# Performance work log

Measured on AMD Instinct MI355X. Metric: run time of the kernel, lower is better.

Reference implementation:

```python
import jax, jax.numpy as jnp
import numpy as np

BS, SL, D, NH = 2, 2048, 1024, 16
HD = D // NH
SCALE = D ** (-0.5)  # NOTE: source scales by full model dim, not head dim


def setup_inputs() -> dict:
    key = jax.random.key(0)
    k1, k2, k3 = jax.random.split(key, 3)
    return {
        "input_sequence": jax.random.normal(k1, (BS, SL, D), dtype=jnp.float32),
        "w_qkv": jax.random.normal(k2, (D, 3 * D), dtype=jnp.float32) * (D ** -0.5),
        "w_out": jax.random.normal(k3, (D, D), dtype=jnp.float32) * (D ** -0.5),
    }


def reference(input_sequence, w_qkv, w_out):
    bs, sl, od = input_sequence.shape
    nh, hd = NH, od // NH
    qkv = input_sequence @ w_qkv                      # [bs, sl, 3d]
    q, k, v = jnp.split(qkv, 3, axis=-1)              # each [bs, sl, d]
    q = q * SCALE

    def heads(x):  # [bs, sl, d] -> [bs, nh, sl, hd]
        return x.reshape(bs, sl, nh, hd).transpose(0, 2, 1, 3)

    q, k, v = heads(q), heads(k), heads(v)
    scores = jnp.einsum("bhqd,bhkd->bhqk", q, k)      # [bs, nh, sl, sl]
    weights = jax.nn.softmax(scores, axis=-1)
    ctx = jnp.einsum("bhqk,bhkd->bhqd", weights, v)   # [bs, nh, sl, hd]
    ctx = ctx.transpose(0, 2, 1, 3).reshape(bs, sl, od)
    return ctx @ w_out
```

## Files before the change

### kernel.cpp

```cpp
#include <hip/hip_runtime.h>
#include <cstdint>
#include <cstddef>

typedef float f32x4 __attribute__((ext_vector_type(4)));
typedef float f32x16 __attribute__((ext_vector_type(16)));
typedef __bf16 bf16x8 __attribute__((ext_vector_type(8)));
typedef __bf16 bf16x4 __attribute__((ext_vector_type(4)));
typedef uint32_t u32x4 __attribute__((ext_vector_type(4)));

static constexpr int BSZ = 2, SL = 2048, DM = 1024, NH = 16, HD = 64;
static constexpr int MROWS = BSZ * SL;
static constexpr float LOG2E = 1.4426950408889634f;
static constexpr float QSCALE = 0.03125f * LOG2E;

__device__ __forceinline__ f32x4 mfma16(bf16x8 a, bf16x8 b, f32x4 c) {
    return __builtin_amdgcn_mfma_f32_16x16x32_bf16(a, b, c, 0, 0, 0);
}
__device__ __forceinline__ f32x16 mfma32(bf16x8 a, bf16x8 b, f32x16 c) {
    return __builtin_amdgcn_mfma_f32_32x32x16_bf16(a, b, c, 0, 0, 0);
}
__device__ __forceinline__ uint32_t pkbf(float lo, float hi) {
    uint16_t a = __builtin_bit_cast(uint16_t, (__bf16)lo);
    uint16_t b = __builtin_bit_cast(uint16_t, (__bf16)hi);
    return ((uint32_t)b << 16) | (uint32_t)a;
}
__device__ __forceinline__ float fexp2(float x) {
#if __has_builtin(__builtin_amdgcn_exp2f)
    return __builtin_amdgcn_exp2f(x);
#else
    float r; asm volatile("v_exp_f32 %0, %1" : "=v"(r) : "v"(x)); return r;
#endif
}
__device__ __forceinline__ void gload16(const void* g, void* l) {
    __builtin_amdgcn_global_load_lds(
        (const __attribute__((address_space(1))) uint32_t*)g,
        (__attribute__((address_space(3))) uint32_t*)l, 16, 0, 0);
}

__global__ __launch_bounds__(256) void r12_cast(const float* __restrict__ in,
                                                __bf16* __restrict__ out, int n) {
    int i = (blockIdx.x * 256 + threadIdx.x) * 4;
    if (i >= n) return;
    float4 v = *(const float4*)&in[i];
    bf16x4 o;
    o.x = (__bf16)v.x; o.y = (__bf16)v.y; o.z = (__bf16)v.z; o.w = (__bf16)v.w;
    *(bf16x4*)&out[i] = o;
}

__global__ __launch_bounds__(256) void r12_transpose_cast(const float* __restrict__ in,
                                                          __bf16* __restrict__ out,
                                                          int R, int C) {
    __shared__ float tile[32][33];
    int c0 = blockIdx.x * 32, r0 = blockIdx.y * 32;
    int tx = threadIdx.x & 31, ty = threadIdx.x >> 5;
#pragma unroll
    for (int i = 0; i < 32; i += 8)
        tile[ty + i][tx] = in[(size_t)(r0 + ty + i) * C + c0 + tx];
    __syncthreads();
#pragma unroll
    for (int i = 0; i < 32; i += 8)
        out[(size_t)(c0 + ty + i) * R + r0 + tx] = (__bf16)tile[tx][ty + i];
}

template <int EPI, int BN>
__global__ __launch_bounds__(256) void r12_gemm(
    const __bf16* __restrict__ A, const __bf16* __restrict__ Bt,
    float* __restrict__ ob, int M, int N, int K,
    __bf16* __restrict__ qb, __bf16* __restrict__ kb, __bf16* __restrict__ vtb)
{
    constexpr int BM = 128, BK = 32;
    constexpr int FN = BN / 32;
    __shared__ __bf16 As[BM * BK];
    __shared__ __bf16 Bs[BN * BK];
    const int tid  = threadIdx.x;
    const int m0   = blockIdx.y * BM, n0 = blockIdx.x * BN;
    const int wave = tid >> 6, lane = tid & 63;
    const int lcol = lane & 15, lgrp = lane >> 4;
    const int wm   = (wave >> 1) * 64, wn = (wave & 1) * (BN / 2);
    const int grow = lane >> 2, gcol = (lane & 3) * 8;

    f32x4 acc[4][FN] = {};

    for (int k0 = 0; k0 < K; k0 += BK) {
        {
            const int cA0 = 2 * wave;
            gload16(&A[(size_t)(m0 + cA0 * 16 + grow) * K + k0 + gcol], &As[cA0 * 512]);
            gload16(&A[(size_t)(m0 + (cA0 + 1) * 16 + grow) * K + k0 + gcol], &As[(cA0 + 1) * 512]);
            if constexpr (BN == 128) {
                gload16(&Bt[(size_t)(n0 + cA0 * 16 + grow) * K + k0 + gcol], &Bs[cA0 * 512]);
                gload16(&Bt[(size_t)(n0 + (cA0 + 1) * 16 + grow) * K + k0 + gcol], &Bs[(cA0 + 1) * 512]);
            } else {
                gload16(&Bt[(size_t)(n0 + wave * 16 + grow) * K + k0 + gcol], &Bs[wave * 512]);
            }
        }
        __syncthreads();
        bf16x8 af[4], bfr[FN];
#pragma unroll
        for (int f = 0; f < 4; ++f)
            af[f] = *(const bf16x8*)&As[(wm + f * 16 + lcol) * BK + lgrp * 8];
#pragma unroll
        for (int f = 0; f < FN; ++f)
            bfr[f] = *(const bf16x8*)&Bs[(wn + f * 16 + lcol) * BK + lgrp * 8];
#pragma unroll
        for (int fm = 0; fm < 4; ++fm)
#pragma unroll
            for (int fn = 0; fn < FN; ++fn)
                acc[fm][fn] = mfma16(af[fm], bfr[fn], acc[fm][fn]);
        __syncthreads();
    }

#pragma unroll
    for (int fm = 0; fm < 4; ++fm) {
#pragma unroll
        for (int fn = 0; fn < FN; ++fn) {
            int n = n0 + wn + fn * 16 + lcol;
#pragma unroll
            for (int r = 0; r < 4; ++r) {
                int m = m0 + wm + fm * 16 + lgrp * 4 + r;
                float v = acc[fm][fn][r];
                if (EPI == 0) {
                    ob[(size_t)m * N + n] = v;
                } else {
                    int sec = n >> 10, nm = n & 1023;
                    int h = nm >> 6, d = nm & 63;
                    int b = m >> 11, s = m & 2047;
                    size_t bh = (size_t)(b * NH + h);
                    if (sec == 0)      qb[(bh * SL + s) * HD + d]  = (__bf16)(v * QSCALE);
                    else if (sec == 1) kb[(bh * SL + s) * HD + d]  = (__bf16)v;
                    else               vtb[(bh * HD + d) * SL + s] = (__bf16)v;
                }
            }
        }
    }
}

#define PV_STEP(a0,a1,a2,a3,a4,a5,a6,a7, KS) do {                               \
    uint32_t w0 = pkbf(a0, a1), w1 = pkbf(a2, a3);                              \
    uint32_t w2 = pkbf(a4, a5), w3 = pkbf(a6, a7);                              \
    asm volatile("v_permlane32_swap_b32 %0, %1" : "+v"(w0), "+v"(w2));          \
    asm volatile("v_permlane32_swap_b32 %0, %1" : "+v"(w1), "+v"(w3));          \
    u32x4 pw = {w0, w1, w2, w3};                                                \
    bf16x8 pf = __builtin_bit_cast(bf16x8, pw);                                 \
    const int cv = (((KS) * 2 + h) ^ swz8) * 8;                                 \
    bf16x8 vf0 = *(const bf16x8*)&Vl[lq * 64 + cv];                             \
    bf16x8 vf1 = *(const bf16x8*)&Vl[(lq + 32) * 64 + cv];                      \
    accT0 = mfma32(vf0, pf, accT0);                                             \
    accT1 = mfma32(vf1, pf, accT1);                                             \
} while (0)

#define TILE_BODY(TI, KA, KB, VA, VB) do {                                      \
    const int cur = (TI) & 1;                                                   \
    {                                                                           \
        __bf16* dK = &arena[cur * 8192 + oA];                                   \
        __bf16* dV = dK + 4096;                                                 \
        *(int4*)dK = KA;  *(int4*)(dK + 2048) = KB;                             \
        *(int4*)dV = VA;  *(int4*)(dV + 2048) = VB;                             \
    }                                                                           \
    if ((TI) + 2 < NT) {                                                        \
        const __bf16* nK = KgA + (size_t)((TI) + 2) * 64 * HD;                  \
        const __bf16* nV = VgA + (size_t)((TI) + 2) * 64;                       \
        KA = *(const int4*)(nK);                                                \
        KB = *(const int4*)(nK + (size_t)32 * HD);                              \
        VA = *(const int4*)(nV);                                                \
        VB = *(const int4*)(nV + (size_t)32 * SL);                              \
    }                                                                           \
    asm volatile("s_waitcnt lgkmcnt(0)" ::: "memory");                          \
    __builtin_amdgcn_s_barrier();                                               \
    __builtin_amdgcn_sched_barrier(0);                                          \
    const __bf16* Kl = &arena[cur * 8192];                                      \
    const __bf16* Vl = Kl + 4096;                                               \
    f32x16 s0 = {}, s1 = {};                                                    \
    __builtin_amdgcn_s_setprio(1);                                              \
    _Pragma("unroll")                                                           \
    for (int t4 = 0; t4 < 4; ++t4) {                                            \
        const int cv = ((t4 * 2 + h) ^ swz8) * 8;                               \
        bf16x8 kf0 = *(const bf16x8*)&Kl[lq * 64 + cv];                         \
        bf16x8 kf1 = *(const bf16x8*)&Kl[(lq + 32) * 64 + cv];                  \
        s0 = mfma32(kf0, qf[t4], s0);                                           \
        s1 = mfma32(kf1, qf[t4], s1);                                           \
    }                                                                           \
    __builtin_amdgcn_s_setprio(0);                                              \
    float p0[16], p1[16];                                                       \
    _Pragma("unroll")                                                           \
    for (int i = 0; i < 16; ++i) { p0[i] = fexp2(s0[i]); p1[i] = fexp2(s1[i]); }\
    __builtin_amdgcn_s_setprio(1);                                              \
    PV_STEP(p0[0], p0[1], p0[2], p0[3], p0[4], p0[5], p0[6], p0[7], 0);         \
    PV_STEP(p0[8], p0[9], p0[10], p0[11], p0[12], p0[13], p0[14], p0[15], 1);   \
    PV_STEP(p1[0], p1[1], p1[2], p1[3], p1[4], p1[5], p1[6], p1[7], 2);         \
    PV_STEP(p1[8], p1[9], p1[10], p1[11], p1[12], p1[13], p1[14], p1[15], 3);   \
    __builtin_amdgcn_s_setprio(0);                                              \
    float a16[16];                                                              \
    _Pragma("unroll")                                                           \
    for (int i = 0; i < 16; ++i) a16[i] = p0[i] + p1[i];                        \
    _Pragma("unroll")                                                           \
    for (int i = 0; i < 8; ++i) a16[i] += a16[i + 8];                           \
    _Pragma("unroll")                                                           \
    for (int i = 0; i < 4; ++i) a16[i] += a16[i + 4];                           \
    float lt = (a16[0] + a16[1]) + (a16[2] + a16[3]);                           \
    lt += __shfl_xor(lt, 32);                                                   \
    l_run += lt;                                                                \
} while (0)

__global__ __launch_bounds__(256) void r12_attn(
    const __bf16* __restrict__ qb, const __bf16* __restrict__ kb,
    const __bf16* __restrict__ vtb, __bf16* __restrict__ ctx)
{
    __shared__ __bf16 arena[16384];
    const int L = blockIdx.x + 16 * blockIdx.y;
    const int xcd = L & 7, j = L >> 3;
    const int bh = xcd * 4 + (j & 3);
    const int qblk = j >> 2;
    const int tid  = threadIdx.x;
    const int wave = tid >> 6, lane = tid & 63;
    const int lq = lane & 31, h = lane >> 5;
    const int swz8 = lq & 7;
    const int q0 = qblk * 128 + wave * 32;

    const __bf16* Q  = qb  + ((size_t)bh * SL + q0) * HD;
    const __bf16* Kg = kb  + (size_t)bh * SL * HD;
    const __bf16* Vg = vtb + (size_t)bh * HD * SL;

    const int rA = tid >> 3, cA = tid & 7;
    const int sA = cA ^ (rA & 7);
    const int oA = rA * 64 + sA * 8;

    bf16x8 qf[4];
#pragma unroll
    for (int t = 0; t < 4; ++t)
        qf[t] = *(const bf16x8*)&Q[(size_t)lq * HD + t * 16 + h * 8];

    f32x16 accT0 = {}, accT1 = {};
    float l_run = 0.f;

    const __bf16* KgA = Kg + (size_t)rA * HD + cA * 8;
    const __bf16* VgA = Vg + (size_t)rA * SL + cA * 8;
    int4 kA0 = *(const int4*)(KgA);
    int4 kB0 = *(const int4*)(KgA + (size_t)32 * HD);
    int4 vA0 = *(const int4*)(VgA);
    int4 vB0 = *(const int4*)(VgA + (size_t)32 * SL);
    int4 kA1 = *(const int4*)(KgA + (size_t)64 * HD);
    int4 kB1 = *(const int4*)(KgA + (size_t)96 * HD);
    int4 vA1 = *(const int4*)(VgA + 64);
    int4 vB1 = *(const int4*)(VgA + (size_t)32 * SL + 64);

    constexpr int NT = SL / 64;
    for (int t = 0; t < NT; t += 2) {
        TILE_BODY(t,     kA0, kB0, vA0, vB0);
        TILE_BODY(t + 1, kA1, kB1, vA1, vB1);
    }

    float inv = 1.f / l_run;
    __syncthreads();
    __bf16* Osw = &arena[wave * 2304];
#pragma unroll
    for (int r = 0; r < 16; ++r) {
        int d0 = (r & 3) + 8 * (r >> 2) + 4 * h;
        Osw[lq * 72 + d0]      = (__bf16)(accT0[r] * inv);
        Osw[lq * 72 + 32 + d0] = (__bf16)(accT1[r] * inv);
    }
    asm volatile("s_waitcnt lgkmcnt(0)" ::: "memory");
    __builtin_amdgcn_sched_barrier(0);
    const int b = bh >> 4, head = bh & 15;
    const int qr = lane >> 1, seg = (lane & 1) * 32;
    __bf16* dst = &ctx[((size_t)b * SL + q0 + qr) * DM + head * HD + seg];
#pragma unroll
    for (int c = 0; c < 4; ++c)
        *(bf16x8*)&dst[c * 8] = *(const bf16x8*)&Osw[qr * 72 + seg + c * 8];
}

extern "C" void kernel_launch(void* const* d_in, const int* in_sizes, int n_in,
                              void* d_out, int out_size, void* d_ws, size_t ws_size,
                              hipStream_t stream) {
    const float* x    = (const float*)d_in[0];
    const float* wqkv = (const float*)d_in[1];
    const float* wout = (const float*)d_in[2];
    float* out = (float*)d_out;

    __bf16* ws    = (__bf16*)d_ws;
    __bf16* xb    = ws;
    __bf16* wqkvT = xb    + (size_t)MROWS * DM;
    __bf16* woutT = wqkvT + (size_t)3 * DM * DM;
    __bf16* qbuf  = woutT + (size_t)DM * DM;
    __bf16* kbuf  = qbuf  + (size_t)MROWS * DM;
    __bf16* vtbuf = kbuf  + (size_t)MROWS * DM;
    __bf16* ctxb  = vtbuf + (size_t)MROWS * DM;

    r12_cast<<<dim3((MROWS * DM) / 1024), dim3(256), 0, stream>>>(x, xb, MROWS * DM);
    r12_transpose_cast<<<dim3(96, 32), dim3(256), 0, stream>>>(wqkv, wqkvT, DM, 3 * DM);
    r12_transpose_cast<<<dim3(32, 32), dim3(256), 0, stream>>>(wout, woutT, DM, DM);

    r12_gemm<1, 128><<<dim3(24, 32), dim3(256), 0, stream>>>(
        xb, wqkvT, (float*)nullptr, MROWS, 3 * DM, DM, qbuf, kbuf, vtbuf);

    r12_attn<<<dim3(16, 32), dim3(256), 0, stream>>>(qbuf, kbuf, vtbuf, ctxb);

    r12_gemm<0, 64><<<dim3(16, 32), dim3(256), 0, stream>>>(
        ctxb, woutT, out, MROWS, DM, DM,
        (__bf16*)nullptr, (__bf16*)nullptr, (__bf16*)nullptr);
}
```

Baseline: 134.4 us.

## Process two 32-row query blocks per wave in attention to reuse K/V fragments

```diff
diff --git a/kernel.cpp b/kernel.cpp
--- a/kernel.cpp
+++ b/kernel.cpp
@@ -37,7 +37,7 @@
         (__attribute__((address_space(3))) uint32_t*)l, 16, 0, 0);
 }
 
-__global__ __launch_bounds__(256) void r12_cast(const float* __restrict__ in,
+__global__ __launch_bounds__(256) void r13_cast(const float* __restrict__ in,
                                                 __bf16* __restrict__ out, int n) {
     int i = (blockIdx.x * 256 + threadIdx.x) * 4;
     if (i >= n) return;
@@ -47,7 +47,7 @@
     *(bf16x4*)&out[i] = o;
 }
 
-__global__ __launch_bounds__(256) void r12_transpose_cast(const float* __restrict__ in,
+__global__ __launch_bounds__(256) void r13_transpose_cast(const float* __restrict__ in,
                                                           __bf16* __restrict__ out,
                                                           int R, int C) {
     __shared__ float tile[32][33];
@@ -63,7 +63,7 @@
 }
 
 template <int EPI, int BN>
-__global__ __launch_bounds__(256) void r12_gemm(
+__global__ __launch_bounds__(256) void r13_gemm(
     const __bf16* __restrict__ A, const __bf16* __restrict__ Bt,
     float* __restrict__ ob, int M, int N, int K,
     __bf16* __restrict__ qb, __bf16* __restrict__ kb, __bf16* __restrict__ vtb)
@@ -134,18 +134,30 @@
     }
 }
 
-#define PV_STEP(a0,a1,a2,a3,a4,a5,a6,a7, KS) do {                               \
-    uint32_t w0 = pkbf(a0, a1), w1 = pkbf(a2, a3);                              \
-    uint32_t w2 = pkbf(a4, a5), w3 = pkbf(a6, a7);                              \
-    asm volatile("v_permlane32_swap_b32 %0, %1" : "+v"(w0), "+v"(w2));          \
-    asm volatile("v_permlane32_swap_b32 %0, %1" : "+v"(w1), "+v"(w3));          \
-    u32x4 pw = {w0, w1, w2, w3};                                                \
-    bf16x8 pf = __builtin_bit_cast(bf16x8, pw);                                 \
+#define PV2(PA, PB, O, KS) do {                                                 \
+    uint32_t a0 = pkbf(PA[(O) + 0], PA[(O) + 1]);                               \
+    uint32_t a1 = pkbf(PA[(O) + 2], PA[(O) + 3]);                               \
+    uint32_t a2 = pkbf(PA[(O) + 4], PA[(O) + 5]);                               \
+    uint32_t a3 = pkbf(PA[(O) + 6], PA[(O) + 7]);                               \
+    asm volatile("v_permlane32_swap_b32 %0, %1" : "+v"(a0), "+v"(a2));          \
+    asm volatile("v_permlane32_swap_b32 %0, %1" : "+v"(a1), "+v"(a3));          \
+    u32x4 wa = {a0, a1, a2, a3};                                                \
+    bf16x8 pfA = __builtin_bit_cast(bf16x8, wa);                                \
+    uint32_t b0 = pkbf(PB[(O) + 0], PB[(O) + 1]);                               \
+    uint32_t b1 = pkbf(PB[(O) + 2], PB[(O) + 3]);                               \
+    uint32_t b2 = pkbf(PB[(O) + 4], PB[(O) + 5]);                               \
+    uint32_t b3 = pkbf(PB[(O) + 6], PB[(O) + 7]);                               \
+    asm volatile("v_permlane32_swap_b32 %0, %1" : "+v"(b0), "+v"(b2));          \
+    asm volatile("v_permlane32_swap_b32 %0, %1" : "+v"(b1), "+v"(b3));          \
+    u32x4 wb = {b0, b1, b2, b3};                                                \
+    bf16x8 pfB = __builtin_bit_cast(bf16x8, wb);                                \
     const int cv = (((KS) * 2 + h) ^ swz8) * 8;                                 \
     bf16x8 vf0 = *(const bf16x8*)&Vl[lq * 64 + cv];                             \
     bf16x8 vf1 = *(const bf16x8*)&Vl[(lq + 32) * 64 + cv];                      \
-    accT0 = mfma32(vf0, pf, accT0);                                             \
-    accT1 = mfma32(vf1, pf, accT1);                                             \
+    accT0 = mfma32(vf0, pfA, accT0);                                            \
+    accT1 = mfma32(vf1, pfA, accT1);                                            \
+    accT2 = mfma32(vf0, pfB, accT2);                                            \
+    accT3 = mfma32(vf1, pfB, accT3);                                            \
 } while (0)
 
 #define TILE_BODY(TI, KA, KB, VA, VB) do {                                      \
@@ -169,44 +181,52 @@
     __builtin_amdgcn_sched_barrier(0);                                          \
     const __bf16* Kl = &arena[cur * 8192];                                      \
     const __bf16* Vl = Kl + 4096;                                               \
-    f32x16 s0 = {}, s1 = {};                                                    \
+    f32x16 sA0 = {}, sA1 = {}, sB0 = {}, sB1 = {};                              \
     __builtin_amdgcn_s_setprio(1);                                              \
     _Pragma("unroll")                                                           \
     for (int t4 = 0; t4 < 4; ++t4) {                                            \
         const int cv = ((t4 * 2 + h) ^ swz8) * 8;                               \
         bf16x8 kf0 = *(const bf16x8*)&Kl[lq * 64 + cv];                         \
         bf16x8 kf1 = *(const bf16x8*)&Kl[(lq + 32) * 64 + cv];                  \
-        s0 = mfma32(kf0, qf[t4], s0);                                           \
-        s1 = mfma32(kf1, qf[t4], s1);                                           \
+        sA0 = mfma32(kf0, qfA[t4], sA0);                                        \
+        sB0 = mfma32(kf0, qfB[t4], sB0);                                        \
+        sA1 = mfma32(kf1, qfA[t4], sA1);                                        \
+        sB1 = mfma32(kf1, qfB[t4], sB1);                                        \
     }                                                                           \
     __builtin_amdgcn_s_setprio(0);                                              \
-    float p0[16], p1[16];                                                       \
-    _Pragma("unroll")                                                           \
-    for (int i = 0; i < 16; ++i) { p0[i] = fexp2(s0[i]); p1[i] = fexp2(s1[i]); }\
+    float pA0[16], pA1[16], pB0[16], pB1[16];                                   \
+    _Pragma("unroll")                                                           \
+    for (int i = 0; i < 16; ++i) {                                              \
+        pA0[i] = fexp2(sA0[i]); pA1[i] = fexp2(sA1[i]);                         \
+        pB0[i] = fexp2(sB0[i]); pB1[i] = fexp2(sB1[i]);                         \
+    }                                                                           \
     __builtin_amdgcn_s_setprio(1);                                              \
-    PV_STEP(p0[0], p0[1], p0[2], p0[3], p0[4], p0[5], p0[6], p0[7], 0);         \
-    PV_STEP(p0[8], p0[9], p0[10], p0[11], p0[12], p0[13], p0[14], p0[15], 1);   \
-    PV_STEP(p1[0], p1[1], p1[2], p1[3], p1[4], p1[5], p1[6], p1[7], 2);         \
-    PV_STEP(p1[8], p1[9], p1[10], p1[11], p1[12], p1[13], p1[14], p1[15], 3);   \
+    PV2(pA0, pB0, 0, 0);                                                        \
+    PV2(pA0, pB0, 8, 1);                                                        \
+    PV2(pA1, pB1, 0, 2);                                                        \
+    PV2(pA1, pB1, 8, 3);                                                        \
     __builtin_amdgcn_s_setprio(0);                                              \
-    float a16[16];                                                              \
-    _Pragma("unroll")                                                           \
-    for (int i = 0; i < 16; ++i) a16[i] = p0[i] + p1[i];                        \
-    _Pragma("unroll")                                                           \
-    for (int i = 0; i < 8; ++i) a16[i] += a16[i + 8];                           \
-    _Pragma("unroll")                                                           \
-    for (int i = 0; i < 4; ++i) a16[i] += a16[i + 4];                           \
-    float lt = (a16[0] + a16[1]) + (a16[2] + a16[3]);                           \
-    lt += __shfl_xor(lt, 32);                                                   \
-    l_run += lt;                                                                \
+    float a16[16], b16[16];                                                     \
+    _Pragma("unroll")                                                           \
+    for (int i = 0; i < 16; ++i) { a16[i] = pA0[i] + pA1[i]; b16[i] = pB0[i] + pB1[i]; } \
+    _Pragma("unroll")                                                           \
+    for (int i = 0; i < 8; ++i) { a16[i] += a16[i + 8]; b16[i] += b16[i + 8]; } \
+    _Pragma("unroll")                                                           \
+    for (int i = 0; i < 4; ++i) { a16[i] += a16[i + 4]; b16[i] += b16[i + 4]; } \
+    float ltA = (a16[0] + a16[1]) + (a16[2] + a16[3]);                          \
+    float ltB = (b16[0] + b16[1]) + (b16[2] + b16[3]);                          \
+    ltA += __shfl_xor(ltA, 32);                                                 \
+    ltB += __shfl_xor(ltB, 32);                                                 \
+    lA += ltA;                                                                  \
+    lB += ltB;                                                                  \
 } while (0)
 
-__global__ __launch_bounds__(256) void r12_attn(
+__global__ __launch_bounds__(256, 1) void r13_attn(
     const __bf16* __restrict__ qb, const __bf16* __restrict__ kb,
     const __bf16* __restrict__ vtb, __bf16* __restrict__ ctx)
 {
     __shared__ __bf16 arena[16384];
-    const int L = blockIdx.x + 16 * blockIdx.y;
+    const int L = blockIdx.x + 8 * blockIdx.y;
     const int xcd = L & 7, j = L >> 3;
     const int bh = xcd * 4 + (j & 3);
     const int qblk = j >> 2;
@@ -214,7 +234,7 @@
     const int wave = tid >> 6, lane = tid & 63;
     const int lq = lane & 31, h = lane >> 5;
     const int swz8 = lq & 7;
-    const int q0 = qblk * 128 + wave * 32;
+    const int q0 = qblk * 256 + wave * 64;
 
     const __bf16* Q  = qb  + ((size_t)bh * SL + q0) * HD;
     const __bf16* Kg = kb  + (size_t)bh * SL * HD;
@@ -224,13 +244,15 @@
     const int sA = cA ^ (rA & 7);
     const int oA = rA * 64 + sA * 8;
 
-    bf16x8 qf[4];
-#pragma unroll
-    for (int t = 0; t < 4; ++t)
-        qf[t] = *(const bf16x8*)&Q[(size_t)lq * HD + t * 16 + h * 8];
-
-    f32x16 accT0 = {}, accT1 = {};
-    float l_run = 0.f;
+    bf16x8 qfA[4], qfB[4];
+#pragma unroll
+    for (int t = 0; t < 4; ++t) {
+        qfA[t] = *(const bf16x8*)&Q[(size_t)lq * HD + t * 16 + h * 8];
+        qfB[t] = *(const bf16x8*)&Q[(size_t)(lq + 32) * HD + t * 16 + h * 8];
+    }
+
+    f32x16 accT0 = {}, accT1 = {}, accT2 = {}, accT3 = {};
+    float lA = 0.f, lB = 0.f;
 
     const __bf16* KgA = Kg + (size_t)rA * HD + cA * 8;
     const __bf16* VgA = Vg + (size_t)rA * SL + cA * 8;
@@ -249,23 +271,41 @@
         TILE_BODY(t + 1, kA1, kB1, vA1, vB1);
     }
 
-    float inv = 1.f / l_run;
+    float invA = 1.f / lA, invB = 1.f / lB;
     __syncthreads();
     __bf16* Osw = &arena[wave * 2304];
+    const int b = bh >> 4, head = bh & 15;
+    const int qr = lane >> 1, seg = (lane & 1) * 32;
 #pragma unroll
     for (int r = 0; r < 16; ++r) {
         int d0 = (r & 3) + 8 * (r >> 2) + 4 * h;
-        Osw[lq * 72 + d0]      = (__bf16)(accT0[r] * inv);
-        Osw[lq * 72 + 32 + d0] = (__bf16)(accT1[r] * inv);
+        Osw[lq * 72 + d0]      = (__bf16)(accT0[r] * invA);
+        Osw[lq * 72 + 32 + d0] = (__bf16)(accT1[r] * invA);
     }
     asm volatile("s_waitcnt lgkmcnt(0)" ::: "memory");
     __builtin_amdgcn_sched_barrier(0);
-    const int b = bh >> 4, head = bh & 15;
-    const int qr = lane >> 1, seg = (lane & 1) * 32;
-    __bf16* dst = &ctx[((size_t)b * SL + q0 + qr) * DM + head * HD + seg];
-#pragma unroll
-    for (int c = 0; c < 4; ++c)
-        *(bf16x8*)&dst[c * 8] = *(const bf16x8*)&Osw[qr * 72 + seg + c * 8];
+    {
+        __bf16* dst = &ctx[((size_t)b * SL + q0 + qr) * DM + head * HD + seg];
+#pragma unroll
+        for (int c = 0; c < 4; ++c)
+            *(bf16x8*)&dst[c * 8] = *(const bf16x8*)&Osw[qr * 72 + seg + c * 8];
+    }
+    asm volatile("s_waitcnt lgkmcnt(0)" ::: "memory");
+    __builtin_amdgcn_sched_barrier(0);
+#pragma unroll
+    for (int r = 0; r < 16; ++r) {
+        int d0 = (r & 3) + 8 * (r >> 2) + 4 * h;
+        Osw[lq * 72 + d0]      = (__bf16)(accT2[r] * invB);
+        Osw[lq * 72 + 32 + d0] = (__bf16)(accT3[r] * invB);
+    }
+    asm volatile("s_waitcnt lgkmcnt(0)" ::: "memory");
+    __builtin_amdgcn_sched_barrier(0);
+    {
+        __bf16* dst = &ctx[((size_t)b * SL + q0 + 32 + qr) * DM + head * HD + seg];
+#pragma unroll
+        for (int c = 0; c < 4; ++c)
+            *(bf16x8*)&dst[c * 8] = *(const bf16x8*)&Osw[qr * 72 + seg + c * 8];
+    }
 }
 
 extern "C" void kernel_launch(void* const* d_in, const int* in_sizes, int n_in,
@@ -285,16 +325,16 @@
     __bf16* vtbuf = kbuf  + (size_t)MROWS * DM;
     __bf16* ctxb  = vtbuf + (size_t)MROWS * DM;
 
-    r12_cast<<<dim3((MROWS * DM) / 1024), dim3(256), 0, stream>>>(x, xb, MROWS * DM);
-    r12_transpose_cast<<<dim3(96, 32), dim3(256), 0, stream>>>(wqkv, wqkvT, DM, 3 * DM);
-    r12_transpose_cast<<<dim3(32, 32), dim3(256), 0, stream>>>(wout, woutT, DM, DM);
-
-    r12_gemm<1, 128><<<dim3(24, 32), dim3(256), 0, stream>>>(
+    r13_cast<<<dim3((MROWS * DM) / 1024), dim3(256), 0, stream>>>(x, xb, MROWS * DM);
+    r13_transpose_cast<<<dim3(96, 32), dim3(256), 0, stream>>>(wqkv, wqkvT, DM, 3 * DM);
+    r13_transpose_cast<<<dim3(32, 32), dim3(256), 0, stream>>>(wout, woutT, DM, DM);
+
+    r13_gemm<1, 128><<<dim3(24, 32), dim3(256), 0, stream>>>(
         xb, wqkvT, (float*)nullptr, MROWS, 3 * DM, DM, qbuf, kbuf, vtbuf);
 
-    r12_attn<<<dim3(16, 32), dim3(256), 0, stream>>>(qbuf, kbuf, vtbuf, ctxb);
-
-    r12_gemm<0, 64><<<dim3(16, 32), dim3(256), 0, stream>>>(
+    r13_attn<<<dim3(8, 32), dim3(256), 0, stream>>>(qbuf, kbuf, vtbuf, ctxb);
+
+    r13_gemm<0, 64><<<dim3(16, 32), dim3(256), 0, stream>>>(
         ctxb, woutT, out, MROWS, DM, DM,
         (__bf16*)nullptr, (__bf16*)nullptr, (__bf16*)nullptr);
 }
```

After: 139.5 us. 3.8% more time.

## Rewrite QKV projection GEMM with 256x256 tiles, double-buffered LDS and XCD remap

Applied to the files above, without the earlier changes.

```diff
diff --git a/kernel.cpp b/kernel.cpp
--- a/kernel.cpp
+++ b/kernel.cpp
@@ -37,7 +37,7 @@
         (__attribute__((address_space(3))) uint32_t*)l, 16, 0, 0);
 }
 
-__global__ __launch_bounds__(256) void r12_cast(const float* __restrict__ in,
+__global__ __launch_bounds__(256) void r17_cast(const float* __restrict__ in,
                                                 __bf16* __restrict__ out, int n) {
     int i = (blockIdx.x * 256 + threadIdx.x) * 4;
     if (i >= n) return;
@@ -47,7 +47,7 @@
     *(bf16x4*)&out[i] = o;
 }
 
-__global__ __launch_bounds__(256) void r12_transpose_cast(const float* __restrict__ in,
+__global__ __launch_bounds__(256) void r17_transpose_cast(const float* __restrict__ in,
                                                           __bf16* __restrict__ out,
                                                           int R, int C) {
     __shared__ float tile[32][33];
@@ -62,11 +62,116 @@
         out[(size_t)(c0 + ty + i) * R + r0 + tx] = (__bf16)tile[tx][ty + i];
 }
 
-template <int EPI, int BN>
-__global__ __launch_bounds__(256) void r12_gemm(
+__global__ __launch_bounds__(512, 2) void r17_gemm1(
     const __bf16* __restrict__ A, const __bf16* __restrict__ Bt,
-    float* __restrict__ ob, int M, int N, int K,
+    int M, int N, int K,
     __bf16* __restrict__ qb, __bf16* __restrict__ kb, __bf16* __restrict__ vtb)
+{
+    __shared__ __bf16 arena[65536];
+    const int L  = blockIdx.x + 12 * blockIdx.y;
+    const int Ls = (L & 7) * 24 + (L >> 3);
+    const int bx = Ls % 12, by = Ls / 12;
+    const int n0 = bx * 256, m0 = by * 256;
+
+    const int tid  = threadIdx.x;
+    const int wave = tid >> 6, lane = tid & 63;
+    const int wr = wave >> 2, wc = wave & 3;
+    const int lcol = lane & 15, lgrp = lane >> 4;
+
+    const int srow = wave * 16 + (lane >> 3);
+    const int slin = lane & 7;
+
+    f32x4 acc[8][4] = {};
+    const int NT = K / 64;
+
+#pragma unroll
+    for (int q = 0; q < 4; ++q) {
+#pragma unroll
+        for (int j = 0; j < 2; ++j) {
+            const int r = srow + j * 8;
+            const int slot = slin ^ (((r >> 2) & 1) << 1);
+            const __bf16* src = (q < 2)
+                ? &A [(size_t)(m0 + q * 128 + r) * K + slot * 8]
+                : &Bt[(size_t)(n0 + (q - 2) * 128 + r) * K + slot * 8];
+            gload16(src, &arena[(q < 2 ? q * 8192 : 16384 + (q - 2) * 8192)
+                                + (wave * 2 + j) * 512]);
+        }
+    }
+    asm volatile("s_waitcnt vmcnt(0)" ::: "memory");
+    __builtin_amdgcn_s_barrier();
+    __builtin_amdgcn_sched_barrier(0);
+
+    for (int t = 0; t < NT; ++t) {
+        const int cur = t & 1;
+        const __bf16* Ab = &arena[cur * 32768];
+        const __bf16* Bb = Ab + 16384;
+        __bf16* dbuf = &arena[(cur ^ 1) * 32768];
+        const int kn = (t + 1) * 64;
+        const bool pf = (t + 1 < NT);
+
+#pragma unroll
+        for (int q = 0; q < 4; ++q) {
+            const int mh = q >> 1, ksub = q & 1;
+            if (pf) {
+#pragma unroll
+                for (int j = 0; j < 2; ++j) {
+                    const int r = srow + j * 8;
+                    const int slot = slin ^ (((r >> 2) & 1) << 1);
+                    const __bf16* src = (q < 2)
+                        ? &A [(size_t)(m0 + q * 128 + r) * K + kn + slot * 8]
+                        : &Bt[(size_t)(n0 + (q - 2) * 128 + r) * K + kn + slot * 8];
+                    gload16(src, dbuf + (q < 2 ? q * 8192 : 16384 + (q - 2) * 8192)
+                                      + (wave * 2 + j) * 512);
+                }
+            }
+            bf16x8 af[4], bfr[4];
+#pragma unroll
+            for (int f = 0; f < 4; ++f) {
+                const int ra = wr * 128 + mh * 64 + f * 16 + lcol;
+                const int ua = (ksub * 4 + lgrp) ^ (((ra >> 2) & 1) << 1);
+                af[f] = *(const bf16x8*)&Ab[ra * 64 + ua * 8];
+                const int rb = wc * 64 + f * 16 + lcol;
+                const int ub = (ksub * 4 + lgrp) ^ (((rb >> 2) & 1) << 1);
+                bfr[f] = *(const bf16x8*)&Bb[rb * 64 + ub * 8];
+            }
+            __builtin_amdgcn_s_setprio(1);
+#pragma unroll
+            for (int fm = 0; fm < 4; ++fm)
+#pragma unroll
+                for (int fn = 0; fn < 4; ++fn)
+                    acc[mh * 4 + fm][fn] = mfma16(af[fm], bfr[fn], acc[mh * 4 + fm][fn]);
+            __builtin_amdgcn_s_setprio(0);
+        }
+        asm volatile("s_waitcnt vmcnt(0)" ::: "memory");
+        __builtin_amdgcn_s_barrier();
+        __builtin_amdgcn_sched_barrier(0);
+    }
+
+#pragma unroll
+    for (int fm = 0; fm < 8; ++fm) {
+#pragma unroll
+        for (int fn = 0; fn < 4; ++fn) {
+            const int n = n0 + wc * 64 + fn * 16 + lcol;
+            const int sec = n >> 10, nm = n & 1023;
+            const int hh = nm >> 6, d = nm & 63;
+#pragma unroll
+            for (int r = 0; r < 4; ++r) {
+                const int m = m0 + wr * 128 + fm * 16 + lgrp * 4 + r;
+                const int b = m >> 11, s = m & 2047;
+                const size_t bh = (size_t)(b * NH + hh);
+                const float v = acc[fm][fn][r];
+                if (sec == 0)      qb[(bh * SL + s) * HD + d]  = (__bf16)(v * QSCALE);
+                else if (sec == 1) kb[(bh * SL + s) * HD + d]  = (__bf16)v;
+                else               vtb[(bh * HD + d) * SL + s] = (__bf16)v;
+            }
+        }
+    }
+}
+
+template <int BN>
+__global__ __launch_bounds__(256) void r17_gemm2(
+    const __bf16* __restrict__ A, const __bf16* __restrict__ Bt,
+    float* __restrict__ ob, int M, int N, int K)
 {
     constexpr int BM = 128, BK = 32;
     constexpr int FN = BN / 32;
@@ -110,28 +215,16 @@
     }
 
 #pragma unroll
-    for (int fm = 0; fm < 4; ++fm) {
+    for (int fm = 0; fm < 4; ++fm)
 #pragma unroll
         for (int fn = 0; fn < FN; ++fn) {
             int n = n0 + wn + fn * 16 + lcol;
 #pragma unroll
             for (int r = 0; r < 4; ++r) {
                 int m = m0 + wm + fm * 16 + lgrp * 4 + r;
-                float v = acc[fm][fn][r];
-                if (EPI == 0) {
-                    ob[(size_t)m * N + n] = v;
-                } else {
-                    int sec = n >> 10, nm = n & 1023;
-                    int h = nm >> 6, d = nm & 63;
-                    int b = m >> 11, s = m & 2047;
-                    size_t bh = (size_t)(b * NH + h);
-                    if (sec == 0)      qb[(bh * SL + s) * HD + d]  = (__bf16)(v * QSCALE);
-                    else if (sec == 1) kb[(bh * SL + s) * HD + d]  = (__bf16)v;
-                    else               vtb[(bh * HD + d) * SL + s] = (__bf16)v;
-                }
-            }
-        }
-    }
+                ob[(size_t)m * N + n] = acc[fm][fn][r];
+            }
+        }
 }
 
 #define PV_STEP(a0,a1,a2,a3,a4,a5,a6,a7, KS) do {                               \
@@ -201,7 +294,7 @@
     l_run += lt;                                                                \
 } while (0)
 
-__global__ __launch_bounds__(256) void r12_attn(
+__global__ __launch_bounds__(256) void r17_attn(
     const __bf16* __restrict__ qb, const __bf16* __restrict__ kb,
     const __bf16* __restrict__ vtb, __bf16* __restrict__ ctx)
 {
@@ -285,16 +378,15 @@
     __bf16* vtbuf = kbuf  + (size_t)MROWS * DM;
     __bf16* ctxb  = vtbuf + (size_t)MROWS * DM;
 
-    r12_cast<<<dim3((MROWS * DM) / 1024), dim3(256), 0, stream>>>(x, xb, MROWS * DM);
-    r12_transpose_cast<<<dim3(96, 32), dim3(256), 0, stream>>>(wqkv, wqkvT, DM, 3 * DM);
-    r12_transpose_cast<<<dim3(32, 32), dim3(256), 0, stream>>>(wout, woutT, DM, DM);
-
-    r12_gemm<1, 128><<<dim3(24, 32), dim3(256), 0, stream>>>(
-        xb, wqkvT, (float*)nullptr, MROWS, 3 * DM, DM, qbuf, kbuf, vtbuf);
-
-    r12_attn<<<dim3(16, 32), dim3(256), 0, stream>>>(qbuf, kbuf, vtbuf, ctxb);
-
-    r12_gemm<0, 64><<<dim3(16, 32), dim3(256), 0, stream>>>(
-        ctxb, woutT, out, MROWS, DM, DM,
-        (__bf16*)nullptr, (__bf16*)nullptr, (__bf16*)nullptr);
-}
+    r17_cast<<<dim3((MROWS * DM) / 1024), dim3(256), 0, stream>>>(x, xb, MROWS * DM);
+    r17_transpose_cast<<<dim3(96, 32), dim3(256), 0, stream>>>(wqkv, wqkvT, DM, 3 * DM);
+    r17_transpose_cast<<<dim3(32, 32), dim3(256), 0, stream>>>(wout, woutT, DM, DM);
+
+    r17_gemm1<<<dim3(12, 16), dim3(512), 0, stream>>>(
+        xb, wqkvT, MROWS, 3 * DM, DM, qbuf, kbuf, vtbuf);
+
+    r17_attn<<<dim3(16, 32), dim3(256), 0, stream>>>(qbuf, kbuf, vtbuf, ctxb);
+
+    r17_gemm2<64><<<dim3(16, 32), dim3(256), 0, stream>>>(
+        ctxb, woutT, out, MROWS, DM, DM);
+}
```

Result: slower. 142.7 us (+6.2%).
